# Kernel optimization log

Measured on AMD Instinct MI355X. Metric: run time of the kernel, lower is better.

Reference implementation:

```python
import jax, jax.numpy as jnp
import numpy as np

FIELD_DIMS = [100000, 1000, 100, 50]
NUM_FEATURES = 12
NUM_CAT = len(FIELD_DIMS)
NUM_CONT = NUM_FEATURES - NUM_CAT
D = 32            # embed_dim
HID = [64, 32]
B, T = 1024, 200
BN_EPS = 1e-5


def setup_inputs() -> dict:
    key = jax.random.key(0)
    ks = jax.random.split(key, 32)
    # x: [B, T, F]; first NUM_CAT cols are integer category ids stored as float
    cat_cols = [jax.random.randint(ks[i], (B, T, 1), 0, FIELD_DIMS[i]).astype(jnp.float32)
                for i in range(NUM_CAT)]
    cont_cols = jax.random.normal(ks[4], (B, T, NUM_CONT), dtype=jnp.float32)
    x = jnp.concatenate(cat_cols + [cont_cols], axis=-1)
    s = 0.05
    inp = {"x": x}
    for i, fd in enumerate(FIELD_DIMS):
        inp[f"emb{i}"] = jax.random.normal(ks[5 + i], (fd, D), dtype=jnp.float32) * s
        inp[f"lin{i}"] = jax.random.normal(ks[9 + i], (fd, D), dtype=jnp.float32) * s
    # Conv1d(1, D, 1) per continuous field == per-field affine map scalar -> D
    inp["cont_w"]  = jax.random.normal(ks[13], (NUM_CONT, D), dtype=jnp.float32) * s
    inp["cont_b"]  = jax.random.normal(ks[14], (NUM_CONT, D), dtype=jnp.float32) * s
    inp["clin_w"]  = jax.random.normal(ks[15], (NUM_CONT, D), dtype=jnp.float32) * s
    inp["clin_b"]  = jax.random.normal(ks[16], (NUM_CONT, D), dtype=jnp.float32) * s
    inp["fin_bias"] = jnp.zeros((D,), dtype=jnp.float32)
    # DNN tower: kernel_size-1 Conv1d == dense over channel dim
    dims = [NUM_FEATURES * D] + HID
    for li in range(len(HID)):
        fan_in = dims[li]
        inp[f"w{li+1}"] = jax.random.normal(ks[17 + 4 * li], (HID[li], fan_in), dtype=jnp.float32) / np.sqrt(fan_in)
        inp[f"b{li+1}"] = jnp.zeros((HID[li],), dtype=jnp.float32)
        inp[f"g{li+1}"] = jnp.ones((HID[li],), dtype=jnp.float32)
        inp[f"beta{li+1}"] = jnp.zeros((HID[li],), dtype=jnp.float32)
    inp["w_out"] = jax.random.normal(ks[30], (D, HID[-1]), dtype=jnp.float32) / np.sqrt(HID[-1])
    inp["b_out"] = jnp.zeros((D,), dtype=jnp.float32)
    return inp


def _batchnorm(h, g, b):
    # training-mode BN over (batch, time), biased variance (torch default)
    mu = h.mean(axis=(0, 1))
    var = h.var(axis=(0, 1))
    return g * (h - mu) * jax.lax.rsqrt(var + BN_EPS) + b


def reference(x, emb0, emb1, emb2, emb3, lin0, lin1, lin2, lin3,
              cont_w, cont_b, clin_w, clin_b, fin_bias,
              w1, b1, g1, beta1, w2, b2, g2, beta2, w_out, b_out):
    embs = [emb0, emb1, emb2, emb3]
    lins = [lin0, lin1, lin2, lin3]
    cat_idx = x[..., :NUM_CAT].astype(jnp.int32)          # [B,T,C]
    xc = x[..., NUM_CAT:]                                  # [B,T,Nc]

    # per-field embeddings -> [B,T,F,D]
    cat_emb = jnp.stack([embs[i][cat_idx[..., i]] for i in range(NUM_CAT)], axis=2)
    cont_emb = xc[..., None] * cont_w + cont_b             # [B,T,Nc,D]
    emb_all = jnp.concatenate([cat_emb, cont_emb], axis=2)  # [B,T,F,D]

    # FM pairwise interaction (sum-of-squares trick)
    s = emb_all.sum(axis=2)                                # [B,T,D]
    interaction = 0.5 * (s * s - (emb_all * emb_all).sum(axis=2))

    # linear terms
    lin_cat = sum(lins[i][cat_idx[..., i]] for i in range(NUM_CAT))      # [B,T,D]
    lin_cont = (xc[..., None] * clin_w + clin_b).sum(axis=2)             # [B,T,D]
    linear = lin_cat + lin_cont + fin_bias

    # DNN tower (k=1 convs == dense over F*D channels); dropout omitted (eval)
    h = emb_all.reshape(B, T, NUM_FEATURES * D)
    h = jax.nn.relu(_batchnorm(h @ w1.T + b1, g1, beta1))
    h = jax.nn.relu(_batchnorm(h @ w2.T + b2, g2, beta2))
    dnn = h @ w_out.T + b_out                              # [B,T,D]

    return linear + interaction + dnn                      # [B,T,D]
```

## Files before the change

kernel.cpp:

```cpp
#include <hip/hip_runtime.h>
#include <hip/hip_bf16.h>

typedef __hip_bfloat16 bf16;

#define ROWS 204800
#define N_INV (1.0f / 204800.0f)

__device__ float g_stats[256];
__device__ bf16  g_E1_0b[100000 * 64];
__device__ float g_E1_1[1000 * 64];
__device__ float g_E1_2[100 * 64];
__device__ float g_E1_3[50 * 64];
__device__ float g_U[8 * 64];
__device__ float g_Vb[64];
__device__ bf16  g_h1p[ROWS * 64];
__device__ bf16  g_h2p[ROWS * 32];

__device__ __forceinline__ int clampi(int v, int hi) {
    return v < 0 ? 0 : (v > hi ? hi : v);
}
__device__ __forceinline__ float rl_f(float v, int l) {
    return __uint_as_float((unsigned int)__builtin_amdgcn_readlane((int)__float_as_uint(v), l));
}
__device__ __forceinline__ float us2f(unsigned short u) {
    return __uint_as_float(((unsigned int)u) << 16);
}

__global__ __launch_bounds__(64) void precompute_kernel(
    const float* __restrict__ emb1, const float* __restrict__ emb2, const float* __restrict__ emb3,
    const float* __restrict__ cont_w, const float* __restrict__ cont_b,
    const float* __restrict__ w1, const float* __restrict__ b1)
{
    int b = blockIdx.x;
    int k = threadIdx.x;
    __shared__ float row[32];

    if (b < 1150) {
        const float* tab; float* out; int i, colOff;
        if (b < 1000)      { tab = emb1; out = g_E1_1; i = b;        colOff = 32; }
        else if (b < 1100) { tab = emb2; out = g_E1_2; i = b - 1000; colOff = 64; }
        else               { tab = emb3; out = g_E1_3; i = b - 1100; colOff = 96; }
        if (k < 32) row[k] = tab[i * 32 + k];
        __syncthreads();
        const float* wr = w1 + k * 384 + colOff;
        float acc = 0.f;
        #pragma unroll
        for (int d = 0; d < 32; ++d) acc = fmaf(row[d], wr[d], acc);
        out[i * 64 + k] = acc;
    } else {
        g_stats[k]       = 0.f;
        g_stats[k + 64]  = 0.f;
        g_stats[k + 128] = 0.f;
        g_stats[k + 192] = 0.f;

        float vb = b1[k];
        #pragma unroll
        for (int j = 0; j < 8; ++j) {
            const float* wr = w1 + k * 384 + (4 + j) * 32;
            float u = 0.f;
            #pragma unroll
            for (int d = 0; d < 32; ++d) {
                float w = wr[d];
                u  = fmaf(cont_w[j * 32 + d], w, u);
                vb = fmaf(cont_b[j * 32 + d], w, vb);
            }
            g_U[j * 64 + k] = u;
        }
        g_Vb[k] = vb;
    }
}

__global__ __launch_bounds__(256) void e10_kernel(
    const float* __restrict__ emb0, const float* __restrict__ w1)
{
    int lane = threadIdx.x & 63;
    int wv   = threadIdx.x >> 6;

    float w1col[32];
    {
        const float4* wr = (const float4*)(w1 + lane * 384);
        #pragma unroll
        for (int q = 0; q < 8; ++q) {
            float4 v = wr[q];
            w1col[4*q+0] = v.x; w1col[4*q+1] = v.y;
            w1col[4*q+2] = v.z; w1col[4*q+3] = v.w;
        }
    }

    for (int i = blockIdx.x * 4 + wv; i < 100000; i += gridDim.x * 4) {
        float e = emb0[i * 32 + (lane & 31)];
        float a0 = 0.f, a1 = 0.f, a2 = 0.f, a3 = 0.f;
        #pragma unroll
        for (int dd = 0; dd < 32; dd += 4) {
            a0 = fmaf(rl_f(e, dd + 0), w1col[dd + 0], a0);
            a1 = fmaf(rl_f(e, dd + 1), w1col[dd + 1], a1);
            a2 = fmaf(rl_f(e, dd + 2), w1col[dd + 2], a2);
            a3 = fmaf(rl_f(e, dd + 3), w1col[dd + 3], a3);
        }
        g_E1_0b[i * 64 + lane] = __float2bfloat16((a0 + a1) + (a2 + a3));
    }
}

__global__ __launch_bounds__(256) void phase1_kernel(
    const float* __restrict__ x,
    const float* __restrict__ emb0, const float* __restrict__ lin0,
    const float* __restrict__ emb1, const float* __restrict__ lin1,
    const float* __restrict__ emb2, const float* __restrict__ lin2,
    const float* __restrict__ emb3, const float* __restrict__ lin3,
    const float* __restrict__ cont_w, const float* __restrict__ cont_b,
    const float* __restrict__ clin_w, const float* __restrict__ clin_b,
    const float* __restrict__ fin_bias,
    float* __restrict__ fm_out)
{
    __shared__ float lsum[64], lsq[64];

    int tid  = threadIdx.x;
    int lane = tid & 63;
    int wv   = tid >> 6;
    int d    = lane & 31;
    bool lo  = lane < 32;

    if (tid < 64) { lsum[tid] = 0.f; lsq[tid] = 0.f; }
    __syncthreads();

    float uk[8];
    #pragma unroll
    for (int j = 0; j < 8; ++j) uk[j] = g_U[j * 64 + lane];
    float vbk = g_Vb[lane];

    float p1[8], p2[8], fb = 0.f;
    if (lo) {
        #pragma unroll
        for (int j = 0; j < 8; ++j) { p1[j] = cont_w[j * 32 + d]; p2[j] = cont_b[j * 32 + d]; }
    } else {
        #pragma unroll
        for (int j = 0; j < 8; ++j) { p1[j] = clin_w[j * 32 + d]; p2[j] = clin_b[j * 32 + d]; }
        fb = fin_bias[d];
    }

    const float* T0 = lo ? emb0 : lin0;
    const float* T1 = lo ? emb1 : lin1;
    const float* T2 = lo ? emb2 : lin2;
    const float* T3 = lo ? emb3 : lin3;

    int gw   = blockIdx.x * 4 + wv;
    int base = gw * 16;

    float xs[4];
    #pragma unroll
    for (int g = 0; g < 4; ++g)
        xs[g] = (lane < 48) ? x[(base + 4 * g) * 12 + lane] : 0.f;

    float ga[2][4], gb[2][4], gc[2][4], gd[2][4], t1[2][4], t2[2][4], t3[2][4];
    unsigned short e0u[2][4];

    auto issue = [&](int g, int s) {
        #pragma unroll
        for (int t = 0; t < 4; ++t) {
            int f  = t * 12;
            int i0 = clampi((int)rl_f(xs[g], f + 0), 99999);
            int i1 = clampi((int)rl_f(xs[g], f + 1), 999);
            int i2 = clampi((int)rl_f(xs[g], f + 2), 99);
            int i3 = clampi((int)rl_f(xs[g], f + 3), 49);
            ga[s][t]  = T0[i0 * 32 + d];
            gb[s][t]  = T1[i1 * 32 + d];
            gc[s][t]  = T2[i2 * 32 + d];
            gd[s][t]  = T3[i3 * 32 + d];
            e0u[s][t] = ((const unsigned short*)g_E1_0b)[i0 * 64 + lane];
            t1[s][t]  = g_E1_1[i1 * 64 + lane];
            t2[s][t]  = g_E1_2[i2 * 64 + lane];
            t3[s][t]  = g_E1_3[i3 * 64 + lane];
        }
    };

    issue(0, 0);

    float ss = 0.f, qq = 0.f;

    #pragma unroll
    for (int g = 0; g < 4; ++g) {
        int s = g & 1;
        if (g < 3) issue(g + 1, (g + 1) & 1);

        #pragma unroll
        for (int t = 0; t < 4; ++t) {
            int r  = base + 4 * g + t;
            int fo = t * 12 + 4;
            float xc[8];
            #pragma unroll
            for (int j = 0; j < 8; ++j) xc[j] = rl_f(xs[g], fo + j);

            float va = ga[s][t], vb = gb[s][t], vc = gc[s][t], vd = gd[s][t];

            float half_val;
            if (lo) {
                float s0 = va + vb, s1 = vc + vd;
                float q0 = fmaf(va, va, vb * vb);
                float q1 = fmaf(vc, vc, vd * vd);
                #pragma unroll
                for (int j = 0; j < 8; ++j) {
                    float ce = fmaf(xc[j], p1[j], p2[j]);
                    if (j & 1) { s1 += ce; q1 = fmaf(ce, ce, q1); }
                    else       { s0 += ce; q0 = fmaf(ce, ce, q0); }
                }
                float sfull = s0 + s1;
                half_val = 0.5f * (sfull * sfull - (q0 + q1));
            } else {
                float l0 = va + vb + fb, l1 = vc + vd;
                #pragma unroll
                for (int j = 0; j < 8; ++j) {
                    if (j & 1) l1 = fmaf(xc[j], p1[j], l1 + p2[j]);
                    else       l0 = fmaf(xc[j], p1[j], l0 + p2[j]);
                }
                half_val = l0 + l1;
            }
            float other = __shfl(half_val, lane | 32);
            if (lo) fm_out[r * 32 + d] = half_val + other;

            float h1 = ((vbk + us2f(e0u[s][t])) + (t1[s][t] + t2[s][t])) + t3[s][t];
            #pragma unroll
            for (int j = 0; j < 8; ++j) h1 = fmaf(xc[j], uk[j], h1);

            g_h1p[r * 64 + lane] = __float2bfloat16(h1);
            ss += h1;
            qq = fmaf(h1, h1, qq);
        }
    }

    atomicAdd(&lsum[lane], ss);
    atomicAdd(&lsq[lane], qq);
    __syncthreads();
    if (tid < 64) {
        atomicAdd(&g_stats[tid], lsum[tid]);
        atomicAdd(&g_stats[64 + tid], lsq[tid]);
    }
}

__global__ __launch_bounds__(256) void phase2_kernel(
    const float* __restrict__ w2, const float* __restrict__ b2,
    const float* __restrict__ g1, const float* __restrict__ beta1)
{
    __shared__ float sa[64], sc[64];
    int tid  = threadIdx.x;
    if (tid < 64) {
        float mu  = g_stats[tid] * N_INV;
        float var = g_stats[64 + tid] * N_INV - mu * mu;
        float a   = g1[tid] * rsqrtf(var + 1e-5f);
        sa[tid] = a;
        sc[tid] = beta1[tid] - a * mu;
    }
    __syncthreads();

    int lane = tid & 63;
    int wv   = tid >> 6;
    size_t row = (size_t)(blockIdx.x * 4 + wv) * 64 + lane;

    const uint4* hrow = (const uint4*)(g_h1p + row * 64);

    float acc[32];
    #pragma unroll
    for (int m = 0; m < 32; ++m) acc[m] = 0.f;

    #pragma unroll
    for (int half = 0; half < 2; ++half) {
        uint4 u[4];
        #pragma unroll
        for (int q = 0; q < 4; ++q) u[q] = hrow[half * 4 + q];

        float y[32];
        #pragma unroll
        for (int q = 0; q < 4; ++q) {
            unsigned int w4[4] = {u[q].x, u[q].y, u[q].z, u[q].w};
            #pragma unroll
            for (int j = 0; j < 4; ++j) {
                int i  = q * 4 + j;
                int ch = half * 32 + 2 * i;
                float f0 = __uint_as_float(w4[j] << 16);
                float f1 = __uint_as_float(w4[j] & 0xffff0000u);
                y[2*i]     = fmaxf(0.f, fmaf(sa[ch],     f0, sc[ch]));
                y[2*i + 1] = fmaxf(0.f, fmaf(sa[ch + 1], f1, sc[ch + 1]));
            }
        }

        #pragma unroll
        for (int m = 0; m < 32; ++m) {
            const float* wr = w2 + m * 64 + half * 32;
            float a0 = 0.f, a1 = 0.f, a2 = 0.f, a3 = 0.f;
            #pragma unroll
            for (int k = 0; k < 32; k += 4) {
                a0 = fmaf(y[k + 0], wr[k + 0], a0);
                a1 = fmaf(y[k + 1], wr[k + 1], a1);
                a2 = fmaf(y[k + 2], wr[k + 2], a2);
                a3 = fmaf(y[k + 3], wr[k + 3], a3);
            }
            acc[m] += (a0 + a1) + (a2 + a3);
        }
    }

    uint4 o[4];
    unsigned int* ow = (unsigned int*)o;
    #pragma unroll
    for (int i = 0; i < 16; ++i) {
        unsigned int lo16 = (unsigned int)__bfloat16_as_ushort(__float2bfloat16(acc[2*i]     + b2[2*i]));
        unsigned int hi16 = (unsigned int)__bfloat16_as_ushort(__float2bfloat16(acc[2*i + 1] + b2[2*i + 1]));
        ow[i] = lo16 | (hi16 << 16);
    }
    uint4* orow = (uint4*)(g_h2p + row * 32);
    #pragma unroll
    for (int q = 0; q < 4; ++q) orow[q] = o[q];
}

__global__ __launch_bounds__(256) void red2_kernel()
{
    __shared__ float ls[64];
    int tid = threadIdx.x;
    if (tid < 64) ls[tid] = 0.f;
    __syncthreads();

    const unsigned int* p = (const unsigned int*)g_h2p;
    int cp = tid & 15;
    float s0 = 0.f, q0 = 0.f, s1 = 0.f, q1 = 0.f;
    for (int i = blockIdx.x * 256 + tid; i < ROWS * 16; i += 256 * 256) {
        unsigned int u = p[i];
        float f0 = __uint_as_float(u << 16);
        float f1 = __uint_as_float(u & 0xffff0000u);
        s0 += f0; q0 = fmaf(f0, f0, q0);
        s1 += f1; q1 = fmaf(f1, f1, q1);
    }
    atomicAdd(&ls[2*cp],      s0);
    atomicAdd(&ls[2*cp + 1],  s1);
    atomicAdd(&ls[32 + 2*cp], q0);
    atomicAdd(&ls[33 + 2*cp], q1);
    __syncthreads();
    if (tid < 32)            atomicAdd(&g_stats[128 + tid], ls[tid]);
    else if (tid < 64)       atomicAdd(&g_stats[160 + (tid - 32)], ls[tid]);
}

__global__ __launch_bounds__(256) void phase3_kernel(
    const float* __restrict__ w_out, const float* __restrict__ b_out,
    const float* __restrict__ g2, const float* __restrict__ beta2,
    float* __restrict__ out)
{
    __shared__ float sa[32], sc[32];
    int tid  = threadIdx.x;
    if (tid < 32) {
        float mu  = g_stats[128 + tid] * N_INV;
        float var = g_stats[160 + tid] * N_INV - mu * mu;
        float a   = g2[tid] * rsqrtf(var + 1e-5f);
        sa[tid] = a;
        sc[tid] = beta2[tid] - a * mu;
    }
    __syncthreads();

    int lane = tid & 63;
    int wv   = tid >> 6;
    size_t row = (size_t)(blockIdx.x * 4 + wv) * 64 + lane;

    const uint4* hrow = (const uint4*)(g_h2p + row * 32);
    uint4 u[4];
    #pragma unroll
    for (int q = 0; q < 4; ++q) u[q] = hrow[q];

    float y2[32];
    #pragma unroll
    for (int q = 0; q < 4; ++q) {
        unsigned int w4[4] = {u[q].x, u[q].y, u[q].z, u[q].w};
        #pragma unroll
        for (int j = 0; j < 4; ++j) {
            int i = q * 4 + j;
            float f0 = __uint_as_float(w4[j] << 16);
            float f1 = __uint_as_float(w4[j] & 0xffff0000u);
            y2[2*i]     = fmaxf(0.f, fmaf(sa[2*i],     f0, sc[2*i]));
            y2[2*i + 1] = fmaxf(0.f, fmaf(sa[2*i + 1], f1, sc[2*i + 1]));
        }
    }

    float res[32];
    #pragma unroll
    for (int dd = 0; dd < 32; ++dd) {
        const float* wr = w_out + dd * 32;
        float a0 = b_out[dd], a1 = 0.f, a2 = 0.f, a3 = 0.f;
        #pragma unroll
        for (int k = 0; k < 32; k += 4) {
            a0 = fmaf(y2[k + 0], wr[k + 0], a0);
            a1 = fmaf(y2[k + 1], wr[k + 1], a1);
            a2 = fmaf(y2[k + 2], wr[k + 2], a2);
            a3 = fmaf(y2[k + 3], wr[k + 3], a3);
        }
        res[dd] = (a0 + a1) + (a2 + a3);
    }

    float4* orow = (float4*)(out + row * 32);
    #pragma unroll
    for (int q = 0; q < 8; ++q) {
        float4 f = orow[q];
        orow[q] = make_float4(res[4*q+0] + f.x, res[4*q+1] + f.y,
                              res[4*q+2] + f.z, res[4*q+3] + f.w);
    }
}

extern "C" void kernel_launch(void* const* d_in, const int* in_sizes, int n_in,
                              void* d_out, int out_size, void* d_ws, size_t ws_size,
                              hipStream_t stream) {
    (void)in_sizes; (void)n_in; (void)out_size; (void)d_ws; (void)ws_size;

    const float* x       = (const float*)d_in[0];
    const float* emb0    = (const float*)d_in[1];
    const float* lin0    = (const float*)d_in[2];
    const float* emb1    = (const float*)d_in[3];
    const float* lin1    = (const float*)d_in[4];
    const float* emb2    = (const float*)d_in[5];
    const float* lin2    = (const float*)d_in[6];
    const float* emb3    = (const float*)d_in[7];
    const float* lin3    = (const float*)d_in[8];
    const float* cont_w  = (const float*)d_in[9];
    const float* cont_b  = (const float*)d_in[10];
    const float* clin_w  = (const float*)d_in[11];
    const float* clin_b  = (const float*)d_in[12];
    const float* fin_bias= (const float*)d_in[13];
    const float* w1      = (const float*)d_in[14];
    const float* b1      = (const float*)d_in[15];
    const float* g1      = (const float*)d_in[16];
    const float* beta1   = (const float*)d_in[17];
    const float* w2      = (const float*)d_in[18];
    const float* b2      = (const float*)d_in[19];
    const float* g2      = (const float*)d_in[20];
    const float* beta2   = (const float*)d_in[21];
    const float* w_out   = (const float*)d_in[22];
    const float* b_out   = (const float*)d_in[23];

    float* outp = (float*)d_out;

    hipLaunchKernelGGL(precompute_kernel, dim3(1151), dim3(64), 0, stream,
                       emb1, emb2, emb3, cont_w, cont_b, w1, b1);

    hipLaunchKernelGGL(e10_kernel, dim3(1600), dim3(256), 0, stream, emb0, w1);

    hipLaunchKernelGGL(phase1_kernel, dim3(3200), dim3(256), 0, stream,
                       x, emb0, lin0, emb1, lin1, emb2, lin2, emb3, lin3,
                       cont_w, cont_b, clin_w, clin_b, fin_bias,
                       outp);

    hipLaunchKernelGGL(phase2_kernel, dim3(800), dim3(256), 0, stream,
                       w2, b2, g1, beta1);

    hipLaunchKernelGGL(red2_kernel, dim3(256), dim3(256), 0, stream);

    hipLaunchKernelGGL(phase3_kernel, dim3(800), dim3(256), 0, stream,
                       w_out, b_out, g2, beta2, outp);
}
```

Measured before the change: 335.9 us.

## Fuse BN2 stats into phase2, store FM output as bf16, pair rows in e10

The separate red2 reduction kernel is removed. Layer-2 batch-norm sums are now computed inside phase2 with wave shuffles and atomics on the fp32 accumulators before they are rounded to bf16. The FM+linear intermediate goes to a bf16 scratch buffer instead of an fp32 read-modify-write of the output, which cuts phase1 writes and phase3 reads. The e10 kernel now handles two embedding rows per wave to use all 64 lanes. The trade is lower precision in the FM term and extra shuffle and atomic work in phase2.

```diff
diff --git a/kernel.cpp b/kernel.cpp
--- a/kernel.cpp
+++ b/kernel.cpp
@@ -15,6 +15,7 @@
 __device__ float g_Vb[64];
 __device__ bf16  g_h1p[ROWS * 64];
 __device__ bf16  g_h2p[ROWS * 32];
+__device__ bf16  g_fmp[ROWS * 32];
 
 __device__ __forceinline__ int clampi(int v, int hi) {
     return v < 0 ? 0 : (v > hi ? hi : v);
@@ -75,6 +76,7 @@
 {
     int lane = threadIdx.x & 63;
     int wv   = threadIdx.x >> 6;
+    int h    = lane >> 5;
 
     float w1col[32];
     {
@@ -87,17 +89,25 @@
         }
     }
 
-    for (int i = blockIdx.x * 4 + wv; i < 100000; i += gridDim.x * 4) {
-        float e = emb0[i * 32 + (lane & 31)];
+    for (int i = blockIdx.x * 8 + wv * 2; i < 100000; i += gridDim.x * 8) {
+        int iA = i, iB = i + 1;
+        float e = emb0[(h ? iB : iA) * 32 + (lane & 31)];
+
         float a0 = 0.f, a1 = 0.f, a2 = 0.f, a3 = 0.f;
+        float b0 = 0.f, b1v = 0.f, b2v = 0.f, b3 = 0.f;
         #pragma unroll
         for (int dd = 0; dd < 32; dd += 4) {
-            a0 = fmaf(rl_f(e, dd + 0), w1col[dd + 0], a0);
-            a1 = fmaf(rl_f(e, dd + 1), w1col[dd + 1], a1);
-            a2 = fmaf(rl_f(e, dd + 2), w1col[dd + 2], a2);
-            a3 = fmaf(rl_f(e, dd + 3), w1col[dd + 3], a3);
-        }
-        g_E1_0b[i * 64 + lane] = __float2bfloat16((a0 + a1) + (a2 + a3));
+            a0  = fmaf(rl_f(e, dd + 0),      w1col[dd + 0], a0);
+            a1  = fmaf(rl_f(e, dd + 1),      w1col[dd + 1], a1);
+            a2  = fmaf(rl_f(e, dd + 2),      w1col[dd + 2], a2);
+            a3  = fmaf(rl_f(e, dd + 3),      w1col[dd + 3], a3);
+            b0  = fmaf(rl_f(e, 32 + dd + 0), w1col[dd + 0], b0);
+            b1v = fmaf(rl_f(e, 32 + dd + 1), w1col[dd + 1], b1v);
+            b2v = fmaf(rl_f(e, 32 + dd + 2), w1col[dd + 2], b2v);
+            b3  = fmaf(rl_f(e, 32 + dd + 3), w1col[dd + 3], b3);
+        }
+        g_E1_0b[iA * 64 + lane] = __float2bfloat16((a0 + a1) + (a2 + a3));
+        g_E1_0b[iB * 64 + lane] = __float2bfloat16((b0 + b1v) + (b2v + b3));
     }
 }
 
@@ -109,8 +119,7 @@
     const float* __restrict__ emb3, const float* __restrict__ lin3,
     const float* __restrict__ cont_w, const float* __restrict__ cont_b,
     const float* __restrict__ clin_w, const float* __restrict__ clin_b,
-    const float* __restrict__ fin_bias,
-    float* __restrict__ fm_out)
+    const float* __restrict__ fin_bias)
 {
     __shared__ float lsum[64], lsq[64];
 
@@ -215,7 +224,7 @@
                 half_val = l0 + l1;
             }
             float other = __shfl(half_val, lane | 32);
-            if (lo) fm_out[r * 32 + d] = half_val + other;
+            if (lo) g_fmp[r * 32 + d] = __float2bfloat16(half_val + other);
 
             float h1 = ((vbk + us2f(e0u[s][t])) + (t1[s][t] + t2[s][t])) + t3[s][t];
             #pragma unroll
@@ -241,6 +250,7 @@
     const float* __restrict__ g1, const float* __restrict__ beta1)
 {
     __shared__ float sa[64], sc[64];
+    __shared__ float ls[64];
     int tid  = threadIdx.x;
     if (tid < 64) {
         float mu  = g_stats[tid] * N_INV;
@@ -248,6 +258,7 @@
         float a   = g1[tid] * rsqrtf(var + 1e-5f);
         sa[tid] = a;
         sc[tid] = beta1[tid] - a * mu;
+        ls[tid] = 0.f;
     }
     __syncthreads();
 
@@ -297,43 +308,45 @@
         }
     }
 
+    #pragma unroll
+    for (int m = 0; m < 32; ++m) acc[m] += b2[m];
+
     uint4 o[4];
     unsigned int* ow = (unsigned int*)o;
     #pragma unroll
     for (int i = 0; i < 16; ++i) {
-        unsigned int lo16 = (unsigned int)__bfloat16_as_ushort(__float2bfloat16(acc[2*i]     + b2[2*i]));
-        unsigned int hi16 = (unsigned int)__bfloat16_as_ushort(__float2bfloat16(acc[2*i + 1] + b2[2*i + 1]));
+        unsigned int lo16 = (unsigned int)__bfloat16_as_ushort(__float2bfloat16(acc[2*i]));
+        unsigned int hi16 = (unsigned int)__bfloat16_as_ushort(__float2bfloat16(acc[2*i + 1]));
         ow[i] = lo16 | (hi16 << 16);
     }
     uint4* orow = (uint4*)(g_h2p + row * 32);
     #pragma unroll
     for (int q = 0; q < 4; ++q) orow[q] = o[q];
-}
-
-__global__ __launch_bounds__(256) void red2_kernel()
-{
-    __shared__ float ls[64];
-    int tid = threadIdx.x;
-    if (tid < 64) ls[tid] = 0.f;
+
+    #pragma unroll
+    for (int c0 = 0; c0 < 32; c0 += 8) {
+        float s[8], q[8];
+        #pragma unroll
+        for (int j = 0; j < 8; ++j) { s[j] = acc[c0 + j]; q[j] = s[j] * s[j]; }
+        #pragma unroll
+        for (int off = 32; off >= 1; off >>= 1) {
+            #pragma unroll
+            for (int j = 0; j < 8; ++j) {
+                s[j] += __shfl_xor(s[j], off);
+                q[j] += __shfl_xor(q[j], off);
+            }
+        }
+        if (lane == 0) {
+            #pragma unroll
+            for (int j = 0; j < 8; ++j) {
+                atomicAdd(&ls[c0 + j],      s[j]);
+                atomicAdd(&ls[32 + c0 + j], q[j]);
+            }
+        }
+    }
     __syncthreads();
-
-    const unsigned int* p = (const unsigned int*)g_h2p;
-    int cp = tid & 15;
-    float s0 = 0.f, q0 = 0.f, s1 = 0.f, q1 = 0.f;
-    for (int i = blockIdx.x * 256 + tid; i < ROWS * 16; i += 256 * 256) {
-        unsigned int u = p[i];
-        float f0 = __uint_as_float(u << 16);
-        float f1 = __uint_as_float(u & 0xffff0000u);
-        s0 += f0; q0 = fmaf(f0, f0, q0);
-        s1 += f1; q1 = fmaf(f1, f1, q1);
-    }
-    atomicAdd(&ls[2*cp],      s0);
-    atomicAdd(&ls[2*cp + 1],  s1);
-    atomicAdd(&ls[32 + 2*cp], q0);
-    atomicAdd(&ls[33 + 2*cp], q1);
-    __syncthreads();
-    if (tid < 32)            atomicAdd(&g_stats[128 + tid], ls[tid]);
-    else if (tid < 64)       atomicAdd(&g_stats[160 + (tid - 32)], ls[tid]);
+    if (tid < 32)       atomicAdd(&g_stats[128 + tid], ls[tid]);
+    else if (tid < 64)  atomicAdd(&g_stats[160 + (tid - 32)], ls[tid]);
 }
 
 __global__ __launch_bounds__(256) void phase3_kernel(
@@ -357,9 +370,10 @@
     size_t row = (size_t)(blockIdx.x * 4 + wv) * 64 + lane;
 
     const uint4* hrow = (const uint4*)(g_h2p + row * 32);
-    uint4 u[4];
-    #pragma unroll
-    for (int q = 0; q < 4; ++q) u[q] = hrow[q];
+    const uint4* frow = (const uint4*)(g_fmp + row * 32);
+    uint4 u[4], fm4[4];
+    #pragma unroll
+    for (int q = 0; q < 4; ++q) { u[q] = hrow[q]; fm4[q] = frow[q]; }
 
     float y2[32];
     #pragma unroll
@@ -375,11 +389,21 @@
         }
     }
 
+    float fmv[32];
+    {
+        const unsigned int* fw = (const unsigned int*)fm4;
+        #pragma unroll
+        for (int i = 0; i < 16; ++i) {
+            fmv[2*i]     = __uint_as_float(fw[i] << 16);
+            fmv[2*i + 1] = __uint_as_float(fw[i] & 0xffff0000u);
+        }
+    }
+
     float res[32];
     #pragma unroll
     for (int dd = 0; dd < 32; ++dd) {
         const float* wr = w_out + dd * 32;
-        float a0 = b_out[dd], a1 = 0.f, a2 = 0.f, a3 = 0.f;
+        float a0 = fmv[dd] + b_out[dd], a1 = 0.f, a2 = 0.f, a3 = 0.f;
         #pragma unroll
         for (int k = 0; k < 32; k += 4) {
             a0 = fmaf(y2[k + 0], wr[k + 0], a0);
@@ -392,11 +416,8 @@
 
     float4* orow = (float4*)(out + row * 32);
     #pragma unroll
-    for (int q = 0; q < 8; ++q) {
-        float4 f = orow[q];
-        orow[q] = make_float4(res[4*q+0] + f.x, res[4*q+1] + f.y,
-                              res[4*q+2] + f.z, res[4*q+3] + f.w);
-    }
+    for (int q = 0; q < 8; ++q)
+        orow[q] = make_float4(res[4*q+0], res[4*q+1], res[4*q+2], res[4*q+3]);
 }
 
 extern "C" void kernel_launch(void* const* d_in, const int* in_sizes, int n_in,
@@ -438,14 +459,11 @@
 
     hipLaunchKernelGGL(phase1_kernel, dim3(3200), dim3(256), 0, stream,
                        x, emb0, lin0, emb1, lin1, emb2, lin2, emb3, lin3,
-                       cont_w, cont_b, clin_w, clin_b, fin_bias,
-                       outp);
+                       cont_w, cont_b, clin_w, clin_b, fin_bias);
 
     hipLaunchKernelGGL(phase2_kernel, dim3(800), dim3(256), 0, stream,
                        w2, b2, g1, beta1);
 
-    hipLaunchKernelGGL(red2_kernel, dim3(256), dim3(256), 0, stream);
-
     hipLaunchKernelGGL(phase3_kernel, dim3(800), dim3(256), 0, stream,
                        w_out, b_out, g2, beta2, outp);
 }
```

After: 328.9 us. -2.1%, faster.
